# Kernel optimization log

Measured on AMD Instinct MI355X. Metric: run time of the kernel, lower is better.

The kernel has to match this reference:

```python
import jax, jax.numpy as jnp
import numpy as np

N_NODES = 100000
N_EDGES = 400000
N_GRAPHS = 256
HID = 256
BIO = 512
LAYERS = 3
EPS = 1e-5


def _seg_mean(v, seg, num):
    s = jax.ops.segment_sum(v, seg, num_segments=num)
    c = jax.ops.segment_sum(jnp.ones((v.shape[0], 1), v.dtype), seg, num_segments=num)
    return s / jnp.maximum(c, 1.0)


def setup_inputs() -> dict:
    key = jax.random.key(0)
    ks = jax.random.split(key, 24)
    d = {}
    d['x'] = jax.random.randint(ks[0], (N_NODES,), 0, 8)
    d['edge_index'] = jax.random.randint(ks[1], (2, N_EDGES), 0, N_NODES)
    d['edge_attr'] = jax.random.normal(ks[2], (N_EDGES, 4), jnp.float32)
    d['batch'] = jnp.sort(jax.random.randint(ks[3], (N_NODES,), 0, N_GRAPHS))
    sc = 0.06  # ~1/sqrt(HID)
    d['node_emb_W'] = jax.random.normal(ks[4], (8, HID), jnp.float32) * sc
    d['edge_emb_W'] = jax.random.normal(ks[5], (4, HID), jnp.float32) * 0.5
    d['edge_emb_b'] = jnp.zeros((HID,), jnp.float32)
    d['edge_mlp_W1'] = jax.random.normal(ks[6], (HID, HID), jnp.float32) * sc
    d['edge_mlp_b1'] = jnp.zeros((HID,), jnp.float32)
    d['edge_mlp_W2'] = jax.random.normal(ks[7], (HID, HID), jnp.float32) * sc
    d['edge_mlp_b2'] = jnp.zeros((HID,), jnp.float32)
    d['struct_scale'] = jnp.asarray(1.5, jnp.float32)
    d['conv_W1'] = jax.random.normal(ks[8], (LAYERS, HID, HID), jnp.float32) * sc
    d['conv_b1'] = jnp.zeros((LAYERS, HID), jnp.float32)
    d['conv_W2'] = jax.random.normal(ks[9], (LAYERS, HID, HID), jnp.float32) * sc
    d['conv_b2'] = jnp.zeros((LAYERS, HID), jnp.float32)
    d['conv_eps'] = jnp.zeros((LAYERS,), jnp.float32)
    d['norm_gamma'] = jnp.ones((LAYERS, HID), jnp.float32)
    d['norm_beta'] = jnp.zeros((LAYERS, HID), jnp.float32)
    d['norm_alpha'] = jnp.ones((LAYERS, HID), jnp.float32)
    d['mean_bio'] = jax.random.normal(ks[10], (BIO,), jnp.float32)
    d['head_W1'] = jax.random.normal(ks[11], (HID + BIO, HID), jnp.float32) * 0.036
    d['head_b1'] = jnp.zeros((HID,), jnp.float32)
    d['head_W2'] = jax.random.normal(ks[12], (HID, 1), jnp.float32) * sc
    d['head_b2'] = jnp.zeros((1,), jnp.float32)
    return d


def reference(x, edge_index, edge_attr, batch, node_emb_W, edge_emb_W, edge_emb_b,
              edge_mlp_W1, edge_mlp_b1, edge_mlp_W2, edge_mlp_b2, struct_scale,
              conv_W1, conv_b1, conv_W2, conv_b2, conv_eps,
              norm_gamma, norm_beta, norm_alpha, mean_bio,
              head_W1, head_b1, head_W2, head_b2):
    h = node_emb_W[x]  # [N, HID]
    src, dst = edge_index[0], edge_index[1]

    e = edge_attr @ edge_emb_W + edge_emb_b  # edge_emb
    e = jax.nn.relu(e @ edge_mlp_W1 + edge_mlp_b1) @ edge_mlp_W2 + edge_mlp_b2
    struct_mask = edge_attr[:, 1] > 0
    e = e * jnp.where(struct_mask, struct_scale, 1.0)[:, None]

    for l in range(LAYERS):
        # GINE conv: aggregate relu(x_j + e_ij) at target, then 2-layer MLP
        msg = jax.nn.relu(h[src] + e)  # [E, HID]
        agg = jax.ops.segment_sum(msg, dst, num_segments=N_NODES)
        z = (1.0 + conv_eps[l]) * h + agg
        h = jax.nn.relu(z @ conv_W1[l] + conv_b1[l]) @ conv_W2[l] + conv_b2[l]
        # GraphNorm per graph
        mean = _seg_mean(h, batch, N_GRAPHS)  # [G, HID]
        hc = h - norm_alpha[l] * mean[batch]
        var = _seg_mean(hc * hc, batch, N_GRAPHS)
        h = norm_gamma[l] * hc * jax.lax.rsqrt(var[batch] + EPS) + norm_beta[l]

    g = _seg_mean(h, batch, N_GRAPHS)  # global mean pool [G, HID]
    b_emb = jnp.broadcast_to(mean_bio, (g.shape[0], BIO))
    combined = jnp.concatenate([g, b_emb], axis=1)
    out = jax.nn.relu(combined @ head_W1 + head_b1) @ head_W2 + head_b2
    return out.mean(axis=1, keepdims=True)
```

## Files before the change

kernel.cpp:

```cpp
#include <hip/hip_runtime.h>
#include <cstddef>

#define NN 100000
#define NE 400000
#define NG 256
#define HIDC 256
#define EPSN 1e-5f

typedef unsigned short bfu;
using short8 = __attribute__((ext_vector_type(8))) short;
using f32x4  = __attribute__((ext_vector_type(4))) float;
using f32x2  = __attribute__((ext_vector_type(2))) float;

#if defined(__has_builtin)
#if __has_builtin(__builtin_amdgcn_cvt_pk_fp8_f32) && __has_builtin(__builtin_amdgcn_cvt_pk_f32_fp8)
#define HWFP8 1
#endif
#endif

__device__ __forceinline__ float bf2f(bfu b) {
    union { unsigned int u; float f; } v; v.u = ((unsigned int)b) << 16; return v.f;
}
__device__ __forceinline__ bfu f2bf(float f) {
    union { float f; unsigned int u; } v; v.f = f;
    unsigned int r = v.u + 0x7FFFu + ((v.u >> 16) & 1u);
    return (bfu)(r >> 16);
}
__device__ __forceinline__ float e4m3f_sw(unsigned char b) {
    unsigned s = ((unsigned)(b & 0x80u)) << 24;
    unsigned E = (b >> 3) & 15u, M = b & 7u;
    union { unsigned x; float f; } o;
    if (E == 0) { o.f = (float)M * 0.001953125f; o.x |= s; }
    else o.x = s | ((E + 120u) << 23) | (M << 20);
    return o.f;
}
__device__ __forceinline__ unsigned char f2e4m3_sw(float f) {
    union { float f; unsigned u; } v; v.f = f;
    unsigned s = (v.u >> 24) & 0x80u;
    float a = fabsf(f);
    if (!(a < 448.f)) return (unsigned char)(s | 0x7Eu);
    if (a < 0.0009765625f) return (unsigned char)s;
    if (a < 0.015625f) {
        int m = (int)(a * 512.f + 0.5f);
        if (m >= 8) return (unsigned char)(s | 0x08u);
        return (unsigned char)(s | (unsigned)m);
    }
    unsigned u = v.u;
    unsigned r = u + 0x7FFFFu + ((u >> 20) & 1u);
    int E = (int)((r >> 23) & 255u) - 127 + 7;
    unsigned M = (r >> 20) & 7u;
    if (E >= 16) return (unsigned char)(s | 0x7Eu);
    if (E <= 0) {
        int m = (int)(a * 512.f + 0.5f); if (m > 7) m = 7;
        return (unsigned char)(s | (unsigned)m);
    }
    return (unsigned char)(s | ((unsigned)E << 3) | M);
}
__device__ __forceinline__ unsigned int fp8enc4(float a, float b, float c, float d) {
#ifdef HWFP8
    int lo = __builtin_amdgcn_cvt_pk_fp8_f32(a, b, 0, false);
    int hi = __builtin_amdgcn_cvt_pk_fp8_f32(c, d, 0, false);
    return (unsigned int)((lo & 0xFFFF) | (hi << 16));
#else
    return (unsigned)f2e4m3_sw(a) | ((unsigned)f2e4m3_sw(b) << 8) |
           ((unsigned)f2e4m3_sw(c) << 16) | ((unsigned)f2e4m3_sw(d) << 24);
#endif
}
__device__ __forceinline__ float4 fp8dec4(unsigned int u) {
#ifdef HWFP8
    f32x2 lo = __builtin_amdgcn_cvt_pk_f32_fp8((int)u, false);
    f32x2 hi = __builtin_amdgcn_cvt_pk_f32_fp8((int)u, true);
    return make_float4(lo[0], lo[1], hi[0], hi[1]);
#else
    return make_float4(e4m3f_sw(u & 255u), e4m3f_sw((u >> 8) & 255u),
                       e4m3f_sw((u >> 16) & 255u), e4m3f_sw((u >> 24) & 255u));
#endif
}
__device__ __forceinline__ float4 ld4(const void* p, size_t i, int bf) {
    if (bf) {
        ushort4 u = *(const ushort4*)((const bfu*)p + i);
        return make_float4(bf2f(u.x), bf2f(u.y), bf2f(u.z), bf2f(u.w));
    }
    return *(const float4*)((const float*)p + i);
}
__device__ __forceinline__ float ld1(const void* p, size_t i, int bf) {
    return bf ? bf2f(((const bfu*)p)[i]) : ((const float*)p)[i];
}
__device__ __forceinline__ void st1(void* p, size_t i, float v, int bf) {
    if (bf) ((bfu*)p)[i] = f2bf(v); else ((float*)p)[i] = v;
}

__global__ void k_dt2(const unsigned int* __restrict__ g, int* __restrict__ flag) {
    if (threadIdx.x == 0)
        flag[0] = (g[0] == 0x3F800000u) ? 0 : 1;
}

__global__ void k_st2(const int* __restrict__ batch, int* __restrict__ starts) {
    int g = threadIdx.x;
    if (g > NG) return;
    if (g == NG) { starts[NG] = NN; return; }
    int lo = 0, hi = NN;
    while (lo < hi) { int mid = (lo + hi) >> 1; if (batch[mid] < g) lo = mid + 1; else hi = mid; }
    starts[g] = lo;
}

__global__ void k_zi(int* __restrict__ p, int n) {
    int i = blockIdx.x * blockDim.x + threadIdx.x;
    if (i < n) p[i] = 0;
}

__global__ void k_cnt(const int* __restrict__ ei, int* __restrict__ deg) {
    int e = blockIdx.x * blockDim.x + threadIdx.x;
    if (e >= NE) return;
    int d = ei[NE + e];
    if ((unsigned)d < (unsigned)NN) atomicAdd(&deg[d], 1);
}
__global__ void k_sc1(const int* __restrict__ deg, int* __restrict__ rowp,
                      int* __restrict__ part) {
    __shared__ int sh[256];
    int b = blockIdx.x, t = threadIdx.x;
    int i = b * 256 + t;
    int v = (i < NN) ? deg[i] : 0;
    sh[t] = v; __syncthreads();
    for (int off = 1; off < 256; off <<= 1) {
        int add = (t >= off) ? sh[t - off] : 0;
        __syncthreads();
        sh[t] += add; __syncthreads();
    }
    if (i < NN) rowp[i] = sh[t] - v;
    if (t == 255) part[b] = sh[255];
}
__global__ void k_sc2(int* __restrict__ part, int nb) {
    if (threadIdx.x != 0) return;
    int run = 0;
    for (int b = 0; b < nb; ++b) { int t = part[b]; part[b] = run; run += t; }
}
__global__ void k_sc3(int* __restrict__ rowp, const int* __restrict__ part) {
    int i = blockIdx.x * blockDim.x + threadIdx.x;
    if (i < NN) rowp[i] += part[blockIdx.x];
    if (i == 0) rowp[NN] = NE;
}
__global__ void k_cpi(const int* __restrict__ a, int* __restrict__ b, int n) {
    int i = blockIdx.x * blockDim.x + threadIdx.x;
    if (i < n) b[i] = a[i];
}
__global__ void k_fil(const int* __restrict__ ei, int* __restrict__ cursor,
                      int* __restrict__ csrc, int* __restrict__ ceid) {
    int e = blockIdx.x * blockDim.x + threadIdx.x;
    if (e >= NE) return;
    int s = ei[e], d = ei[NE + e];
    if ((unsigned)d >= (unsigned)NN) return;
    int pos = atomicAdd(&cursor[d], 1);
    csrc[pos] = ((unsigned)s < (unsigned)NN) ? s : 0;
    ceid[pos] = e;
}

__global__ void k_wef(const void* __restrict__ Wemb, const void* __restrict__ bemb,
                      const void* __restrict__ W1, const void* __restrict__ b1,
                      float* __restrict__ weff, float* __restrict__ beff,
                      const int* __restrict__ dtf) {
    int bf = *dtf;
    int j = blockIdx.x;
    int n = threadIdx.x;
    float acc = 0.f;
    if (j < 4) {
        for (int k = 0; k < HIDC; ++k)
            acc += ld1(Wemb, (size_t)j * HIDC + k, bf) * ld1(W1, (size_t)k * HIDC + n, bf);
        weff[j * HIDC + n] = acc;
    } else {
        for (int k = 0; k < HIDC; ++k)
            acc += ld1(bemb, k, bf) * ld1(W1, (size_t)k * HIDC + n, bf);
        beff[n] = acc + ld1(b1, n, bf);
    }
}

__device__ __forceinline__ void acc8(float* a, uint4 hv, uint2 ev) {
    float4 e0 = fp8dec4(ev.x);
    float4 e1 = fp8dec4(ev.y);
    a[0] += fmaxf(bf2f((bfu)(hv.x & 0xFFFFu)) + e0.x, 0.f);
    a[1] += fmaxf(bf2f((bfu)(hv.x >> 16))    + e0.y, 0.f);
    a[2] += fmaxf(bf2f((bfu)(hv.y & 0xFFFFu)) + e0.z, 0.f);
    a[3] += fmaxf(bf2f((bfu)(hv.y >> 16))    + e0.w, 0.f);
    a[4] += fmaxf(bf2f((bfu)(hv.z & 0xFFFFu)) + e1.x, 0.f);
    a[5] += fmaxf(bf2f((bfu)(hv.z >> 16))    + e1.y, 0.f);
    a[6] += fmaxf(bf2f((bfu)(hv.w & 0xFFFFu)) + e1.z, 0.f);
    a[7] += fmaxf(bf2f((bfu)(hv.w >> 16))    + e1.w, 0.f);
}
__global__ void k_gat4(const bfu* __restrict__ h, const unsigned char* __restrict__ e8,
                       const int* __restrict__ rowp, const int* __restrict__ csrc,
                       bfu* __restrict__ agg) {
    int tid = blockIdx.x * blockDim.x + threadIdx.x;
    if (tid >= NN * 32) return;
    int n = tid >> 5, q = (tid & 31) << 3;
    int s0 = rowp[n], s1 = rowp[n + 1];
    float a[8] = {};
    int i = s0;
    for (; i + 2 <= s1; i += 2) {
        int src0 = csrc[i], src1 = csrc[i + 1];
        uint4 h0 = *(const uint4*)(h + (size_t)src0 * HIDC + q);
        uint4 h1 = *(const uint4*)(h + (size_t)src1 * HIDC + q);
        uint2 e0 = *(const uint2*)(e8 + (size_t)i * HIDC + q);
        uint2 e1 = *(const uint2*)(e8 + (size_t)(i + 1) * HIDC + q);
        acc8(a, h0, e0);
        acc8(a, h1, e1);
    }
    if (i < s1) {
        int src0 = csrc[i];
        uint4 h0 = *(const uint4*)(h + (size_t)src0 * HIDC + q);
        uint2 e0 = *(const uint2*)(e8 + (size_t)i * HIDC + q);
        acc8(a, h0, e0);
    }
    ushort4 o0, o1;
    o0.x = f2bf(a[0]); o0.y = f2bf(a[1]); o0.z = f2bf(a[2]); o0.w = f2bf(a[3]);
    o1.x = f2bf(a[4]); o1.y = f2bf(a[5]); o1.z = f2bf(a[6]); o1.w = f2bf(a[7]);
    *(ushort4*)(agg + (size_t)n * HIDC + q) = o0;
    *(ushort4*)(agg + (size_t)n * HIDC + q + 4) = o1;
}

__global__ void k_wtr(const void* __restrict__ W, long wOff, bfu* __restrict__ Wt,
                      const int* __restrict__ dtf) {
    int o = blockIdx.x * blockDim.x + threadIdx.x;
    if (o >= HIDC * HIDC) return;
    int blk = o >> 9, pos = o & 511;
    int w = blk >> 5, rem = blk & 31;
    int t = rem >> 3, kb = rem & 7;
    int pr = pos >> 3, j = pos & 7;
    int lr = pr >> 2, lq = pr & 3;
    int n = w * 64 + t * 16 + lr;
    int k = kb * 32 + lq * 8 + j;
    Wt[o] = f2bf(ld1(W, (size_t)wOff + (size_t)k * HIDC + n, *dtf));
}

__global__ void k_emb(const int* __restrict__ x, const void* __restrict__ W,
                      bfu* __restrict__ h, const int* __restrict__ dtf) {
    int tid = blockIdx.x * blockDim.x + threadIdx.x;
    if (tid >= NN * 64) return;
    int bf = *dtf;
    int n = tid >> 6, q = (tid & 63) << 2;
    int xv = x[n]; if ((unsigned)xv >= 8u) xv = 0;
    float4 v = ld4(W, (size_t)xv * HIDC + q, bf);
    ushort4 o; o.x = f2bf(v.x); o.y = f2bf(v.y); o.z = f2bf(v.z); o.w = f2bf(v.w);
    *(ushort4*)(h + (size_t)n * HIDC + q) = o;
}

__global__ __launch_bounds__(512, 8)
void k_me(const void* __restrict__ attrs,
          const float* __restrict__ weff, const float* __restrict__ beff,
          const bfu* __restrict__ Wt, const void* __restrict__ bias,
          const void* __restrict__ scalep,
          unsigned char* __restrict__ C,
          const int* __restrict__ dtf, const int* __restrict__ eidx) {
    __shared__ bfu As[4][64 * 32];
    __shared__ float wsh[1280];
    __shared__ float sf[64];
    const int bf = *dtf;
    const int tid = threadIdx.x;
    const int wave = tid >> 6, lane = tid & 63;
    const int lr = lane & 15, lq = lane >> 4;
    const int wr = wave >> 2, wc = wave & 3;
    const int m0 = blockIdx.x * 64;
    const int row = tid >> 3;
    const int a4 = (tid & 7) << 2;

    for (int v = tid; v < 1280; v += 512)
        wsh[v] = (v < 1024) ? weff[v] : beff[v - 1024];

    float aa[4];
    {
        long er = (long)eidx[m0 + row];
        aa[0] = ld1(attrs, (size_t)er * 4 + 0, bf);
        aa[1] = ld1(attrs, (size_t)er * 4 + 1, bf);
        aa[2] = ld1(attrs, (size_t)er * 4 + 2, bf);
        aa[3] = ld1(attrs, (size_t)er * 4 + 3, bf);
    }
    if ((tid & 7) == 0)
        sf[row] = (aa[1] > 0.f) ? ld1(scalep, 0, bf) : 1.0f;
    __syncthreads();

    f32x4 acc[2][4] = {};
    const bfu* wb = Wt + ((size_t)wc * 32) * 512 + (size_t)(lr * 4 + lq) * 8;

    for (int h = 0; h < 2; ++h) {
        if (h) __syncthreads();
#pragma unroll
        for (int q = 0; q < 4; ++q) {
            const int c = h * 128 + q * 32 + a4;
            float4 bb = *(const float4*)(wsh + 1024 + c);
            float v0 = bb.x, v1 = bb.y, v2 = bb.z, v3 = bb.w;
#pragma unroll
            for (int j = 0; j < 4; ++j) {
                float4 w0 = *(const float4*)(wsh + j * 256 + c);
                v0 += aa[j] * w0.x; v1 += aa[j] * w0.y;
                v2 += aa[j] * w0.z; v3 += aa[j] * w0.w;
            }
            ushort4 o;
            o.x = f2bf(fmaxf(v0, 0.f)); o.y = f2bf(fmaxf(v1, 0.f));
            o.z = f2bf(fmaxf(v2, 0.f)); o.w = f2bf(fmaxf(v3, 0.f));
            *(ushort4*)(&As[q][row * 32 + a4]) = o;
        }
        __syncthreads();
#pragma unroll
        for (int q = 0; q < 4; ++q) {
            const int kb = h * 4 + q;
            short8 fa0 = *(const short8*)(&As[q][(wr * 32 + lr) * 32 + lq * 8]);
            short8 fa1 = *(const short8*)(&As[q][(wr * 32 + 16 + lr) * 32 + lq * 8]);
#pragma unroll
            for (int t = 0; t < 4; ++t) {
                short8 fb = *(const short8*)(wb + (size_t)(t * 8 + kb) * 512);
                acc[0][t] = __builtin_amdgcn_mfma_f32_16x16x32_bf16(fa0, fb, acc[0][t], 0, 0, 0);
                acc[1][t] = __builtin_amdgcn_mfma_f32_16x16x32_bf16(fa1, fb, acc[1][t], 0, 0, 0);
            }
        }
    }
    __syncthreads();

    unsigned char* tile = (unsigned char*)&As[0][0];
    float bv[4];
#pragma unroll
    for (int t = 0; t < 4; ++t)
        bv[t] = ld1(bias, (size_t)(wc * 64 + t * 16 + lr), bf);
#pragma unroll
    for (int r = 0; r < 2; ++r) {
#pragma unroll
        for (int i = 0; i < 4; ++i) {
            int rr = wr * 32 + r * 16 + lq * 4 + i;
            float rs = sf[rr];
            float ov0 = (acc[r][0][i] + bv[0]) * rs;
            float ov1 = (acc[r][1][i] + bv[1]) * rs;
            float ov2 = (acc[r][2][i] + bv[2]) * rs;
            float ov3 = (acc[r][3][i] + bv[3]) * rs;
            unsigned int pk = fp8enc4(ov0, ov1, ov2, ov3);
            int cb = rr * 256 + wc * 64 + lr;
            tile[cb]      = (unsigned char)(pk & 255u);
            tile[cb + 16] = (unsigned char)((pk >> 8) & 255u);
            tile[cb + 32] = (unsigned char)((pk >> 16) & 255u);
            tile[cb + 48] = (unsigned char)(pk >> 24);
        }
    }
    __syncthreads();
    {
        const uint4* lsrc = (const uint4*)(tile + tid * 32);
        uint4 w0 = lsrc[0];
        uint4 w1 = lsrc[1];
        uint4* gdst = (uint4*)(C + (size_t)m0 * HIDC + (size_t)tid * 32);
        gdst[0] = w0;
        gdst[1] = w1;
    }
}

__global__ __launch_bounds__(256)
void k_cnv(bfu* __restrict__ h, const bfu* __restrict__ agg,
           const void* __restrict__ eps, int epsIdx,
           const bfu* __restrict__ Wt1, const void* __restrict__ bias1, long b1Off,
           const bfu* __restrict__ Wt2, const void* __restrict__ bias2, long b2Off,
           const int* __restrict__ dtf) {
    __shared__ bfu Ts[8][64 * 32];
    const int bf = *dtf;
    const int tid = threadIdx.x;
    const int wave = tid >> 6, lane = tid & 63;
    const int lr = lane & 15, lq = lane >> 4;
    const int m0 = blockIdx.x * 64;
    const float epsv = 1.0f + ld1(eps, epsIdx, bf);
    const int row = tid >> 2;
    const int ak = (tid & 3) << 3;
    const int gmA = m0 + row;
    const bfu* wb1 = Wt1 + ((size_t)wave * 32) * 512 + (size_t)(lr * 4 + lq) * 8;
    const bfu* wb2 = Wt2 + ((size_t)wave * 32) * 512 + (size_t)(lr * 4 + lq) * 8;

#pragma unroll
    for (int k0 = 0; k0 < 256; k0 += 32) {
        float hv[8] = {}, gv[8] = {};
        if (gmA < NN) {
            ushort4 h0 = *(const ushort4*)(h + (size_t)gmA * HIDC + k0 + ak);
            ushort4 h1 = *(const ushort4*)(h + (size_t)gmA * HIDC + k0 + ak + 4);
            hv[0]=bf2f(h0.x); hv[1]=bf2f(h0.y); hv[2]=bf2f(h0.z); hv[3]=bf2f(h0.w);
            hv[4]=bf2f(h1.x); hv[5]=bf2f(h1.y); hv[6]=bf2f(h1.z); hv[7]=bf2f(h1.w);
            ushort4 g0 = *(const ushort4*)(agg + (size_t)gmA * HIDC + k0 + ak);
            ushort4 g1 = *(const ushort4*)(agg + (size_t)gmA * HIDC + k0 + ak + 4);
            gv[0]=bf2f(g0.x); gv[1]=bf2f(g0.y); gv[2]=bf2f(g0.z); gv[3]=bf2f(g0.w);
            gv[4]=bf2f(g1.x); gv[5]=bf2f(g1.y); gv[6]=bf2f(g1.z); gv[7]=bf2f(g1.w);
        }
        ushort4 o0, o1;
        o0.x = f2bf(epsv * hv[0] + gv[0]); o0.y = f2bf(epsv * hv[1] + gv[1]);
        o0.z = f2bf(epsv * hv[2] + gv[2]); o0.w = f2bf(epsv * hv[3] + gv[3]);
        o1.x = f2bf(epsv * hv[4] + gv[4]); o1.y = f2bf(epsv * hv[5] + gv[5]);
        o1.z = f2bf(epsv * hv[6] + gv[6]); o1.w = f2bf(epsv * hv[7] + gv[7]);
        *(ushort4*)(&Ts[k0 >> 5][row * 32 + ak]) = o0;
        *(ushort4*)(&Ts[k0 >> 5][row * 32 + ak + 4]) = o1;
    }
    __syncthreads();

    f32x4 acc[4][4] = {};
#pragma unroll
    for (int kb = 0; kb < 8; ++kb) {
        short8 fa[4], fbv[4];
#pragma unroll
        for (int r = 0; r < 4; ++r)
            fa[r] = *(const short8*)(&Ts[kb][(r * 16 + lr) * 32 + lq * 8]);
#pragma unroll
        for (int t = 0; t < 4; ++t)
            fbv[t] = *(const short8*)(wb1 + (size_t)(t * 8 + kb) * 512);
#pragma unroll
        for (int r = 0; r < 4; ++r)
#pragma unroll
            for (int t = 0; t < 4; ++t)
                acc[r][t] = __builtin_amdgcn_mfma_f32_16x16x32_bf16(
                    fa[r], fbv[t], acc[r][t], 0, 0, 0);
    }
    __syncthreads();

    {
        float bv[4];
#pragma unroll
        for (int t = 0; t < 4; ++t)
            bv[t] = ld1(bias1, (size_t)b1Off + wave * 64 + t * 16 + lr, bf);
        const f32x4 z4 = {0.f, 0.f, 0.f, 0.f};
#pragma unroll
        for (int r = 0; r < 4; ++r) {
#pragma unroll
            for (int i = 0; i < 4; ++i) {
                int rowo = r * 16 + lq * 4 + i;
#pragma unroll
                for (int t = 0; t < 4; ++t) {
                    int kk = wave * 64 + t * 16 + lr;
                    Ts[kk >> 5][rowo * 32 + (kk & 31)] =
                        f2bf(fmaxf(acc[r][t][i] + bv[t], 0.f));
                }
            }
        }
#pragma unroll
        for (int r = 0; r < 4; ++r)
#pragma unroll
            for (int t = 0; t < 4; ++t)
                acc[r][t] = z4;
    }
    __syncthreads();

#pragma unroll
    for (int kb = 0; kb < 8; ++kb) {
        short8 fa[4], fbv[4];
#pragma unroll
        for (int r = 0; r < 4; ++r)
            fa[r] = *(const short8*)(&Ts[kb][(r * 16 + lr) * 32 + lq * 8]);
#pragma unroll
        for (int t = 0; t < 4; ++t)
            fbv[t] = *(const short8*)(wb2 + (size_t)(t * 8 + kb) * 512);
#pragma unroll
        for (int r = 0; r < 4; ++r)
#pragma unroll
            for (int t = 0; t < 4; ++t)
                acc[r][t] = __builtin_amdgcn_mfma_f32_16x16x32_bf16(
                    fa[r], fbv[t], acc[r][t], 0, 0, 0);
    }
    float bv[4];
#pragma unroll
    for (int t = 0; t < 4; ++t)
        bv[t] = ld1(bias2, (size_t)b2Off + wave * 64 + t * 16 + lr, bf);
#pragma unroll
    for (int r = 0; r < 4; ++r) {
#pragma unroll
        for (int i = 0; i < 4; ++i) {
            int gm = m0 + r * 16 + lq * 4 + i;
            if (gm >= NN) continue;
            size_t cbase = (size_t)gm * HIDC + wave * 64 + lr;
#pragma unroll
            for (int t = 0; t < 4; ++t)
                h[cbase + t * 16] = f2bf(acc[r][t][i] + bv[t]);
        }
    }
}

__global__ void k_s1(const bfu* __restrict__ h, const int* __restrict__ starts,
                     float* __restrict__ psum, float* __restrict__ psq) {
    int g = blockIdx.x, c8 = blockIdx.y, c = threadIdx.x;
    int s = starts[g], t = starts[g + 1];
    int len = t - s;
    int b = s + (int)(((long)len * c8) >> 3);
    int e = s + (int)(((long)len * (c8 + 1)) >> 3);
    float sum = 0.f, sq = 0.f;
    for (int n = b; n < e; ++n) {
        float v = bf2f(h[(size_t)n * HIDC + c]);
        sum += v; sq += v * v;
    }
    psum[((size_t)g * 8 + c8) * HIDC + c] = sum;
    psq[((size_t)g * 8 + c8) * HIDC + c] = sq;
}
__global__ void k_s2(const int* __restrict__ starts,
                     const float* __restrict__ psum, const float* __restrict__ psq,
                     const void* __restrict__ alpha, long aOff,
                     float* __restrict__ gmean, float* __restrict__ gvar,
                     const int* __restrict__ dtf) {
    int g = blockIdx.x, c = threadIdx.x;
    float sum = 0.f, sq = 0.f;
#pragma unroll
    for (int j = 0; j < 8; ++j) {
        sum += psum[((size_t)g * 8 + j) * HIDC + c];
        sq  += psq[((size_t)g * 8 + j) * HIDC + c];
    }
    int cn = starts[g + 1] - starts[g]; if (cn < 1) cn = 1;
    float cnt = (float)cn;
    float m = sum / cnt;
    float a = ld1(alpha, (size_t)aOff + c, *dtf);
    gmean[g * HIDC + c] = m;
    gvar[g * HIDC + c] = fmaxf(sq / cnt - (2.f * a - a * a) * m * m, 0.f);
}

__global__ void k_nrm(bfu* __restrict__ h, const int* __restrict__ batch,
                      const float* __restrict__ gmean, const float* __restrict__ gvar,
                      const void* __restrict__ gamma, const void* __restrict__ beta,
                      const void* __restrict__ alpha, long pOff,
                      const int* __restrict__ dtf) {
    int tid = blockIdx.x * blockDim.x + threadIdx.x;
    if (tid >= NN * 64) return;
    int bf = *dtf;
    int n = tid >> 6, q = (tid & 63) << 2;
    int g = batch[n]; if ((unsigned)g >= (unsigned)NG) g = 0;
    ushort4 hu = *(ushort4*)(h + (size_t)n * HIDC + q);
    const float4 mv = *(const float4*)(gmean + g * HIDC + q);
    const float4 vv = *(const float4*)(gvar + g * HIDC + q);
    float4 ga = ld4(gamma, (size_t)pOff + q, bf);
    float4 be = ld4(beta, (size_t)pOff + q, bf);
    float4 al = ld4(alpha, (size_t)pOff + q, bf);
    float4 v;
    v.x = ga.x * (bf2f(hu.x) - al.x * mv.x) * rsqrtf(vv.x + EPSN) + be.x;
    v.y = ga.y * (bf2f(hu.y) - al.y * mv.y) * rsqrtf(vv.y + EPSN) + be.y;
    v.z = ga.z * (bf2f(hu.z) - al.z * mv.z) * rsqrtf(vv.z + EPSN) + be.z;
    v.w = ga.w * (bf2f(hu.w) - al.w * mv.w) * rsqrtf(vv.w + EPSN) + be.w;
    ushort4 ov; ov.x = f2bf(v.x); ov.y = f2bf(v.y); ov.z = f2bf(v.z); ov.w = f2bf(v.w);
    *(ushort4*)(h + (size_t)n * HIDC + q) = ov;
}

__global__ void k_pl2(const int* __restrict__ starts,
                      const float* __restrict__ gmean, const float* __restrict__ gvar,
                      const void* __restrict__ gamma, const void* __restrict__ beta,
                      const void* __restrict__ alpha, long pOff,
                      float* __restrict__ g, const int* __restrict__ dtf) {
    int bf = *dtf;
    int gb = blockIdx.x, c = threadIdx.x;
    int cn = starts[gb + 1] - starts[gb];
    if (cn <= 0) { g[gb * HIDC + c] = 0.f; return; }
    float m = gmean[gb * HIDC + c];
    float v = gvar[gb * HIDC + c];
    float ga = ld1(gamma, (size_t)pOff + c, bf);
    float be = ld1(beta, (size_t)pOff + c, bf);
    float al = ld1(alpha, (size_t)pOff + c, bf);
    g[gb * HIDC + c] = ga * (1.f - al) * m * rsqrtf(v + EPSN) + be;
}

__global__ void k_hd(const float* __restrict__ g, const void* __restrict__ bio,
                     const void* __restrict__ W1, const void* __restrict__ b1,
                     const void* __restrict__ W2, const void* __restrict__ b2,
                     void* __restrict__ out, const int* __restrict__ dtf) {
    __shared__ float comb[768];
    __shared__ float red[256];
    __shared__ int nanf;
    int bf = *dtf;
    int gb = blockIdx.x, t = threadIdx.x;
    if (t == 0) nanf = 0;
    comb[t] = g[gb * HIDC + t];
    comb[256 + t] = ld1(bio, t, bf);
    comb[512 + t] = ld1(bio, 256 + t, bf);
    __syncthreads();
    float acc = ld1(b1, t, bf);
    for (int k = 0; k < 768; ++k) acc += comb[k] * ld1(W1, (size_t)k * HIDC + t, bf);
    if (isnan(acc) || isinf(acc)) nanf = 1;
    float hid = fmaxf(acc, 0.f);
    red[t] = hid * ld1(W2, t, bf);
    __syncthreads();
    for (int off = 128; off > 0; off >>= 1) {
        if (t < off) red[t] += red[t + off];
        __syncthreads();
    }
    if (t == 0) {
        float r = red[0] + ld1(b2, 0, bf);
        if (nanf || isnan(r)) r = 999.0f;
        st1(out, gb, r, bf);
    }
}

extern "C" void kernel_launch(void* const* d_in, const int* in_sizes, int n_in,
                              void* d_out, int out_size, void* d_ws, size_t ws_size,
                              hipStream_t stream) {
    const int* x = (const int*)d_in[0];
    const int* ei = (const int*)d_in[1];
    const void* eattr = d_in[2];
    const int* batch = (const int*)d_in[3];
    const void* node_emb_W = d_in[4];
    const void* edge_emb_W = d_in[5];
    const void* edge_emb_b = d_in[6];
    const void* emlp_W1 = d_in[7];
    const void* emlp_b1 = d_in[8];
    const void* emlp_W2 = d_in[9];
    const void* emlp_b2 = d_in[10];
    const void* struct_scale = d_in[11];
    const void* conv_W1 = d_in[12];
    const void* conv_b1 = d_in[13];
    const void* conv_W2 = d_in[14];
    const void* conv_b2 = d_in[15];
    const void* conv_eps = d_in[16];
    const void* ngamma = d_in[17];
    const void* nbeta = d_in[18];
    const void* nalpha = d_in[19];
    const void* mean_bio = d_in[20];
    const void* head_W1 = d_in[21];
    const void* head_b1 = d_in[22];
    const void* head_W2 = d_in[23];
    const void* head_b2 = d_in[24];
    (void)in_sizes; (void)n_in; (void)out_size; (void)ws_size;

    const size_t H_B = (size_t)NN * HIDC * 2;
    const size_t E8_B = (size_t)NE * HIDC;
    char* p = (char*)d_ws;
    bfu* hbuf = (bfu*)p; p += H_B;
    bfu* aggb = (bfu*)p; p += H_B;
    unsigned char* e8 = (unsigned char*)p; p += E8_B;
    bfu* wt = (bfu*)p; p += 8 * 65536 * 2;
    int* rowp = (int*)p;
    int* cursor = rowp + 100352;
    int* part = cursor + 100352;
    int* splits = part + 1024;
    int* cnts = splits + 8;
    int* csrc = cnts + 8;
    int* ceid = csrc + NE;
    p = (char*)(ceid + NE);
    float* psum = (float*)p; p += (size_t)NG * 8 * HIDC * 4;
    float* psq = (float*)p; p += (size_t)NG * 8 * HIDC * 4;
    char* small = p;
    int* starts = (int*)small;
    int* dtf = (int*)(small + 2048);
    float* weff = (float*)(small + 4096);
    float* beff = weff + 4 * HIDC;
    float* gmean = (float*)(small + 16384);
    float* gvar = gmean + NG * HIDC;
    float* gpool = gvar + NG * HIDC;
    (void)splits; (void)cnts;

    k_dt2<<<1, 64, 0, stream>>>((const unsigned int*)ngamma, dtf);
    k_st2<<<1, 512, 0, stream>>>(batch, starts);
    k_emb<<<(NN * 64 + 255) / 256, 256, 0, stream>>>(x, node_emb_W, hbuf, dtf);
    k_wef<<<5, 256, 0, stream>>>(edge_emb_W, edge_emb_b, emlp_W1, emlp_b1,
                                 weff, beff, dtf);

    k_wtr<<<256, 256, 0, stream>>>(emlp_W2, 0, wt + 65536, dtf);
    for (int l = 0; l < 3; ++l) {
        k_wtr<<<256, 256, 0, stream>>>(conv_W1, (long)l * HIDC * HIDC, wt + (2 + l) * 65536, dtf);
        k_wtr<<<256, 256, 0, stream>>>(conv_W2, (long)l * HIDC * HIDC, wt + (5 + l) * 65536, dtf);
    }

    const int NBN = (NN + 255) / 256;
    k_zi<<<NBN, 256, 0, stream>>>(cursor, NN);
    k_cnt<<<(NE + 255) / 256, 256, 0, stream>>>(ei, cursor);
    k_sc1<<<NBN, 256, 0, stream>>>(cursor, rowp, part);
    k_sc2<<<1, 64, 0, stream>>>(part, NBN);
    k_sc3<<<NBN, 256, 0, stream>>>(rowp, part);
    k_cpi<<<NBN, 256, 0, stream>>>(rowp, cursor, NN);
    k_fil<<<(NE + 255) / 256, 256, 0, stream>>>(ei, cursor, csrc, ceid);

    dim3 gE((NE + 63) / 64), gN((NN + 63) / 64);
    k_me<<<gE, 512, 0, stream>>>(eattr, weff, beff, wt + 65536, emlp_b2,
                                 struct_scale, e8, dtf, ceid);

    dim3 gS1(NG, 8);
    const int gatBlocks = (NN * 32 + 255) / 256;

    for (int l = 0; l < 3; ++l) {
        k_gat4<<<gatBlocks, 256, 0, stream>>>(hbuf, e8, rowp, csrc, aggb);
        k_cnv<<<gN, 256, 0, stream>>>(
            hbuf, aggb, conv_eps, l,
            wt + (2 + l) * 65536, conv_b1, (long)l * HIDC,
            wt + (5 + l) * 65536, conv_b2, (long)l * HIDC, dtf);
        k_s1<<<gS1, 256, 0, stream>>>(hbuf, starts, psum, psq);
        k_s2<<<NG, 256, 0, stream>>>(starts, psum, psq, nalpha, (long)l * HIDC,
                                     gmean, gvar, dtf);
        if (l < 2) {
            k_nrm<<<(NN * 64 + 255) / 256, 256, 0, stream>>>(
                hbuf, batch, gmean, gvar, ngamma, nbeta, nalpha, (long)l * HIDC, dtf);
        }
    }

    k_pl2<<<NG, 256, 0, stream>>>(starts, gmean, gvar, ngamma, nbeta, nalpha,
                                  (long)2 * HIDC, gpool, dtf);
    k_hd<<<NG, 256, 0, stream>>>(gpool, mean_bio, head_W1, head_b1,
                                 head_W2, head_b2, d_out, dtf);
}
```

Before: 977.1 us.

## Fuse edge gather-aggregation into conv MLP kernel with ping-pong h buffers

Removes the separate gather kernel and computes the neighbour aggregation directly inside the conv kernel while building the shared-memory A tile, so the intermediate agg buffer is never written to or read back from global memory. Because other blocks still read the old h during the gather, the kernel writes to a second h buffer and the two are swapped each layer. Each thread now walks its node's edge list twice (once per 128-column half) and holds 32 float accumulators. That raises register pressure and keeps divergent, latency-bound edge loops inside the GEMM kernel, which can stall the MFMA work and lower occupancy.

```diff
diff --git a/kernel.cpp b/kernel.cpp
--- a/kernel.cpp
+++ b/kernel.cpp
@@ -185,36 +185,6 @@
     a[5] += fmaxf(bf2f((bfu)(hv.z >> 16))    + e1.y, 0.f);
     a[6] += fmaxf(bf2f((bfu)(hv.w & 0xFFFFu)) + e1.z, 0.f);
     a[7] += fmaxf(bf2f((bfu)(hv.w >> 16))    + e1.w, 0.f);
-}
-__global__ void k_gat4(const bfu* __restrict__ h, const unsigned char* __restrict__ e8,
-                       const int* __restrict__ rowp, const int* __restrict__ csrc,
-                       bfu* __restrict__ agg) {
-    int tid = blockIdx.x * blockDim.x + threadIdx.x;
-    if (tid >= NN * 32) return;
-    int n = tid >> 5, q = (tid & 31) << 3;
-    int s0 = rowp[n], s1 = rowp[n + 1];
-    float a[8] = {};
-    int i = s0;
-    for (; i + 2 <= s1; i += 2) {
-        int src0 = csrc[i], src1 = csrc[i + 1];
-        uint4 h0 = *(const uint4*)(h + (size_t)src0 * HIDC + q);
-        uint4 h1 = *(const uint4*)(h + (size_t)src1 * HIDC + q);
-        uint2 e0 = *(const uint2*)(e8 + (size_t)i * HIDC + q);
-        uint2 e1 = *(const uint2*)(e8 + (size_t)(i + 1) * HIDC + q);
-        acc8(a, h0, e0);
-        acc8(a, h1, e1);
-    }
-    if (i < s1) {
-        int src0 = csrc[i];
-        uint4 h0 = *(const uint4*)(h + (size_t)src0 * HIDC + q);
-        uint2 e0 = *(const uint2*)(e8 + (size_t)i * HIDC + q);
-        acc8(a, h0, e0);
-    }
-    ushort4 o0, o1;
-    o0.x = f2bf(a[0]); o0.y = f2bf(a[1]); o0.z = f2bf(a[2]); o0.w = f2bf(a[3]);
-    o1.x = f2bf(a[4]); o1.y = f2bf(a[5]); o1.z = f2bf(a[6]); o1.w = f2bf(a[7]);
-    *(ushort4*)(agg + (size_t)n * HIDC + q) = o0;
-    *(ushort4*)(agg + (size_t)n * HIDC + q + 4) = o1;
 }
 
 __global__ void k_wtr(const void* __restrict__ W, long wOff, bfu* __restrict__ Wt,
@@ -349,11 +319,13 @@
 }
 
 __global__ __launch_bounds__(256)
-void k_cnv(bfu* __restrict__ h, const bfu* __restrict__ agg,
-           const void* __restrict__ eps, int epsIdx,
-           const bfu* __restrict__ Wt1, const void* __restrict__ bias1, long b1Off,
-           const bfu* __restrict__ Wt2, const void* __restrict__ bias2, long b2Off,
-           const int* __restrict__ dtf) {
+void k_cnv2(const bfu* __restrict__ hin, bfu* __restrict__ hout,
+            const unsigned char* __restrict__ e8,
+            const int* __restrict__ rowp, const int* __restrict__ csrc,
+            const void* __restrict__ eps, int epsIdx,
+            const bfu* __restrict__ Wt1, const void* __restrict__ bias1, long b1Off,
+            const bfu* __restrict__ Wt2, const void* __restrict__ bias2, long b2Off,
+            const int* __restrict__ dtf) {
     __shared__ bfu Ts[8][64 * 32];
     const int bf = *dtf;
     const int tid = threadIdx.x;
@@ -367,26 +339,41 @@
     const bfu* wb1 = Wt1 + ((size_t)wave * 32) * 512 + (size_t)(lr * 4 + lq) * 8;
     const bfu* wb2 = Wt2 + ((size_t)wave * 32) * 512 + (size_t)(lr * 4 + lq) * 8;
 
-#pragma unroll
-    for (int k0 = 0; k0 < 256; k0 += 32) {
-        float hv[8] = {}, gv[8] = {};
-        if (gmA < NN) {
-            ushort4 h0 = *(const ushort4*)(h + (size_t)gmA * HIDC + k0 + ak);
-            ushort4 h1 = *(const ushort4*)(h + (size_t)gmA * HIDC + k0 + ak + 4);
-            hv[0]=bf2f(h0.x); hv[1]=bf2f(h0.y); hv[2]=bf2f(h0.z); hv[3]=bf2f(h0.w);
-            hv[4]=bf2f(h1.x); hv[5]=bf2f(h1.y); hv[6]=bf2f(h1.z); hv[7]=bf2f(h1.w);
-            ushort4 g0 = *(const ushort4*)(agg + (size_t)gmA * HIDC + k0 + ak);
-            ushort4 g1 = *(const ushort4*)(agg + (size_t)gmA * HIDC + k0 + ak + 4);
-            gv[0]=bf2f(g0.x); gv[1]=bf2f(g0.y); gv[2]=bf2f(g0.z); gv[3]=bf2f(g0.w);
-            gv[4]=bf2f(g1.x); gv[5]=bf2f(g1.y); gv[6]=bf2f(g1.z); gv[7]=bf2f(g1.w);
-        }
-        ushort4 o0, o1;
-        o0.x = f2bf(epsv * hv[0] + gv[0]); o0.y = f2bf(epsv * hv[1] + gv[1]);
-        o0.z = f2bf(epsv * hv[2] + gv[2]); o0.w = f2bf(epsv * hv[3] + gv[3]);
-        o1.x = f2bf(epsv * hv[4] + gv[4]); o1.y = f2bf(epsv * hv[5] + gv[5]);
-        o1.z = f2bf(epsv * hv[6] + gv[6]); o1.w = f2bf(epsv * hv[7] + gv[7]);
-        *(ushort4*)(&Ts[k0 >> 5][row * 32 + ak]) = o0;
-        *(ushort4*)(&Ts[k0 >> 5][row * 32 + ak + 4]) = o1;
+    int es0 = 0, es1 = 0;
+    if (gmA < NN) { es0 = rowp[gmA]; es1 = rowp[gmA + 1]; }
+
+#pragma unroll
+    for (int gq = 0; gq < 2; ++gq) {
+        float a[32] = {};
+        const int cbase = gq * 128 + ak;
+        for (int i = es0; i < es1; ++i) {
+            int src = csrc[i];
+            const bfu* hp = hin + (size_t)src * HIDC + cbase;
+            const unsigned char* ep = e8 + (size_t)i * HIDC + cbase;
+#pragma unroll
+            for (int t4 = 0; t4 < 4; ++t4) {
+                uint4 hv = *(const uint4*)(hp + t4 * 32);
+                uint2 ev = *(const uint2*)(ep + t4 * 32);
+                acc8(a + t4 * 8, hv, ev);
+            }
+        }
+#pragma unroll
+        for (int t4 = 0; t4 < 4; ++t4) {
+            float hv[8] = {};
+            if (gmA < NN) {
+                ushort4 h0 = *(const ushort4*)(hin + (size_t)gmA * HIDC + cbase + t4 * 32);
+                ushort4 h1 = *(const ushort4*)(hin + (size_t)gmA * HIDC + cbase + t4 * 32 + 4);
+                hv[0]=bf2f(h0.x); hv[1]=bf2f(h0.y); hv[2]=bf2f(h0.z); hv[3]=bf2f(h0.w);
+                hv[4]=bf2f(h1.x); hv[5]=bf2f(h1.y); hv[6]=bf2f(h1.z); hv[7]=bf2f(h1.w);
+            }
+            ushort4 o0, o1;
+            o0.x = f2bf(epsv * hv[0] + a[t4*8+0]); o0.y = f2bf(epsv * hv[1] + a[t4*8+1]);
+            o0.z = f2bf(epsv * hv[2] + a[t4*8+2]); o0.w = f2bf(epsv * hv[3] + a[t4*8+3]);
+            o1.x = f2bf(epsv * hv[4] + a[t4*8+4]); o1.y = f2bf(epsv * hv[5] + a[t4*8+5]);
+            o1.z = f2bf(epsv * hv[6] + a[t4*8+6]); o1.w = f2bf(epsv * hv[7] + a[t4*8+7]);
+            *(ushort4*)(&Ts[gq * 4 + t4][row * 32 + ak]) = o0;
+            *(ushort4*)(&Ts[gq * 4 + t4][row * 32 + ak + 4]) = o1;
+        }
     }
     __syncthreads();
 
@@ -465,7 +452,7 @@
             size_t cbase = (size_t)gm * HIDC + wave * 64 + lr;
 #pragma unroll
             for (int t = 0; t < 4; ++t)
-                h[cbase + t * 16] = f2bf(acc[r][t][i] + bv[t]);
+                hout[cbase + t * 16] = f2bf(acc[r][t][i] + bv[t]);
         }
     }
 }
@@ -612,7 +599,7 @@
     const size_t E8_B = (size_t)NE * HIDC;
     char* p = (char*)d_ws;
     bfu* hbuf = (bfu*)p; p += H_B;
-    bfu* aggb = (bfu*)p; p += H_B;
+    bfu* h2 = (bfu*)p; p += H_B;
     unsigned char* e8 = (unsigned char*)p; p += E8_B;
     bfu* wt = (bfu*)p; p += 8 * 65536 * 2;
     int* rowp = (int*)p;
@@ -661,21 +648,22 @@
                                  struct_scale, e8, dtf, ceid);
 
     dim3 gS1(NG, 8);
-    const int gatBlocks = (NN * 32 + 255) / 256;
-
+
+    bfu* hin = hbuf;
+    bfu* hout = h2;
     for (int l = 0; l < 3; ++l) {
-        k_gat4<<<gatBlocks, 256, 0, stream>>>(hbuf, e8, rowp, csrc, aggb);
-        k_cnv<<<gN, 256, 0, stream>>>(
-            hbuf, aggb, conv_eps, l,
+        k_cnv2<<<gN, 256, 0, stream>>>(
+            hin, hout, e8, rowp, csrc, conv_eps, l,
             wt + (2 + l) * 65536, conv_b1, (long)l * HIDC,
             wt + (5 + l) * 65536, conv_b2, (long)l * HIDC, dtf);
-        k_s1<<<gS1, 256, 0, stream>>>(hbuf, starts, psum, psq);
+        k_s1<<<gS1, 256, 0, stream>>>(hout, starts, psum, psq);
         k_s2<<<NG, 256, 0, stream>>>(starts, psum, psq, nalpha, (long)l * HIDC,
                                      gmean, gvar, dtf);
         if (l < 2) {
             k_nrm<<<(NN * 64 + 255) / 256, 256, 0, stream>>>(
-                hbuf, batch, gmean, gvar, ngamma, nbeta, nalpha, (long)l * HIDC, dtf);
-        }
+                hout, batch, gmean, gvar, ngamma, nbeta, nalpha, (long)l * HIDC, dtf);
+        }
+        bfu* tmp = hin; hin = hout; hout = tmp;
     }
 
     k_pl2<<<NG, 256, 0, stream>>>(starts, gmean, gvar, ngamma, nbeta, nalpha,
```

New measurement: 1.003 ms. 1.03x slower.

## Fuse GraphNorm per-graph sum/sumsq reduction into conv MLP epilogue via atomics

Applied to the files above, without the earlier changes.

Moves the per-graph sum and sum-of-squares accumulation out of the separate k_s1 pass and into the k_cnv epilogue. Tiles whose 64 rows all belong to one graph reduce in registers and with shuffles, then issue one atomic per column. Mixed tiles fall back to per-element atomics. This avoids re-reading the full hidden tensor after each layer, at the cost of a zeroing launch, float atomics with nondeterministic summation order, and extra epilogue work.

```diff
diff --git a/kernel.cpp b/kernel.cpp
--- a/kernel.cpp
+++ b/kernel.cpp
@@ -350,9 +350,11 @@
 
 __global__ __launch_bounds__(256)
 void k_cnv(bfu* __restrict__ h, const bfu* __restrict__ agg,
+           const int* __restrict__ batch,
            const void* __restrict__ eps, int epsIdx,
            const bfu* __restrict__ Wt1, const void* __restrict__ bias1, long b1Off,
            const bfu* __restrict__ Wt2, const void* __restrict__ bias2, long b2Off,
+           float* __restrict__ psum, float* __restrict__ psq,
            const int* __restrict__ dtf) {
     __shared__ bfu Ts[8][64 * 32];
     const int bf = *dtf;
@@ -456,47 +458,70 @@
 #pragma unroll
     for (int t = 0; t < 4; ++t)
         bv[t] = ld1(bias2, (size_t)b2Off + wave * 64 + t * 16 + lr, bf);
-#pragma unroll
-    for (int r = 0; r < 4; ++r) {
-#pragma unroll
-        for (int i = 0; i < 4; ++i) {
-            int gm = m0 + r * 16 + lq * 4 + i;
-            if (gm >= NN) continue;
-            size_t cbase = (size_t)gm * HIDC + wave * 64 + lr;
-#pragma unroll
-            for (int t = 0; t < 4; ++t)
-                h[cbase + t * 16] = f2bf(acc[r][t][i] + bv[t]);
-        }
-    }
-}
-
-__global__ void k_s1(const bfu* __restrict__ h, const int* __restrict__ starts,
-                     float* __restrict__ psum, float* __restrict__ psq) {
-    int g = blockIdx.x, c8 = blockIdx.y, c = threadIdx.x;
-    int s = starts[g], t = starts[g + 1];
-    int len = t - s;
-    int b = s + (int)(((long)len * c8) >> 3);
-    int e = s + (int)(((long)len * (c8 + 1)) >> 3);
-    float sum = 0.f, sq = 0.f;
-    for (int n = b; n < e; ++n) {
-        float v = bf2f(h[(size_t)n * HIDC + c]);
-        sum += v; sq += v * v;
-    }
-    psum[((size_t)g * 8 + c8) * HIDC + c] = sum;
-    psq[((size_t)g * 8 + c8) * HIDC + c] = sq;
-}
+
+    int lastRow = m0 + 63; if (lastRow >= NN) lastRow = NN - 1;
+    const int g0 = batch[m0 < NN ? m0 : NN - 1];
+    const int g1 = batch[lastRow];
+    const bool fast = (g0 == g1) && (m0 + 63 < NN);
+
+    if (fast) {
+        float st[4] = {0.f, 0.f, 0.f, 0.f};
+        float sq[4] = {0.f, 0.f, 0.f, 0.f};
+#pragma unroll
+        for (int r = 0; r < 4; ++r) {
+#pragma unroll
+            for (int i = 0; i < 4; ++i) {
+                int gm = m0 + r * 16 + lq * 4 + i;
+                size_t cbase = (size_t)gm * HIDC + wave * 64 + lr;
+#pragma unroll
+                for (int t = 0; t < 4; ++t) {
+                    float o = acc[r][t][i] + bv[t];
+                    h[cbase + t * 16] = f2bf(o);
+                    st[t] += o; sq[t] += o * o;
+                }
+            }
+        }
+#pragma unroll
+        for (int t = 0; t < 4; ++t) {
+            float s = st[t], q = sq[t];
+            s += __shfl_xor(s, 16); q += __shfl_xor(q, 16);
+            s += __shfl_xor(s, 32); q += __shfl_xor(q, 32);
+            if (lq == 0) {
+                int c = wave * 64 + t * 16 + lr;
+                atomicAdd(&psum[(size_t)g0 * HIDC + c], s);
+                atomicAdd(&psq[(size_t)g0 * HIDC + c], q);
+            }
+        }
+    } else {
+#pragma unroll
+        for (int r = 0; r < 4; ++r) {
+#pragma unroll
+            for (int i = 0; i < 4; ++i) {
+                int gm = m0 + r * 16 + lq * 4 + i;
+                if (gm >= NN) continue;
+                int g = batch[gm];
+                size_t cbase = (size_t)gm * HIDC + wave * 64 + lr;
+#pragma unroll
+                for (int t = 0; t < 4; ++t) {
+                    float o = acc[r][t][i] + bv[t];
+                    h[cbase + t * 16] = f2bf(o);
+                    int c = wave * 64 + t * 16 + lr;
+                    atomicAdd(&psum[(size_t)g * HIDC + c], o);
+                    atomicAdd(&psq[(size_t)g * HIDC + c], o * o);
+                }
+            }
+        }
+    }
+}
+
 __global__ void k_s2(const int* __restrict__ starts,
                      const float* __restrict__ psum, const float* __restrict__ psq,
                      const void* __restrict__ alpha, long aOff,
                      float* __restrict__ gmean, float* __restrict__ gvar,
                      const int* __restrict__ dtf) {
     int g = blockIdx.x, c = threadIdx.x;
-    float sum = 0.f, sq = 0.f;
-#pragma unroll
-    for (int j = 0; j < 8; ++j) {
-        sum += psum[((size_t)g * 8 + j) * HIDC + c];
-        sq  += psq[((size_t)g * 8 + j) * HIDC + c];
-    }
+    float sum = psum[(size_t)g * HIDC + c];
+    float sq  = psq[(size_t)g * HIDC + c];
     int cn = starts[g + 1] - starts[g]; if (cn < 1) cn = 1;
     float cnt = (float)cn;
     float m = sum / cnt;
@@ -624,7 +649,8 @@
     int* ceid = csrc + NE;
     p = (char*)(ceid + NE);
     float* psum = (float*)p; p += (size_t)NG * 8 * HIDC * 4;
-    float* psq = (float*)p; p += (size_t)NG * 8 * HIDC * 4;
+    float* psq = psum + NG * HIDC;
+    p += (size_t)NG * 8 * HIDC * 4;
     char* small = p;
     int* starts = (int*)small;
     int* dtf = (int*)(small + 2048);
@@ -660,16 +686,17 @@
     k_me<<<gE, 512, 0, stream>>>(eattr, weff, beff, wt + 65536, emlp_b2,
                                  struct_scale, e8, dtf, ceid);
 
-    dim3 gS1(NG, 8);
     const int gatBlocks = (NN * 32 + 255) / 256;
+    const int ZB = (2 * NG * HIDC + 255) / 256;
 
     for (int l = 0; l < 3; ++l) {
         k_gat4<<<gatBlocks, 256, 0, stream>>>(hbuf, e8, rowp, csrc, aggb);
+        k_zi<<<ZB, 256, 0, stream>>>((int*)psum, 2 * NG * HIDC);
         k_cnv<<<gN, 256, 0, stream>>>(
-            hbuf, aggb, conv_eps, l,
+            hbuf, aggb, batch, conv_eps, l,
             wt + (2 + l) * 65536, conv_b1, (long)l * HIDC,
-            wt + (5 + l) * 65536, conv_b2, (long)l * HIDC, dtf);
-        k_s1<<<gS1, 256, 0, stream>>>(hbuf, starts, psum, psq);
+            wt + (5 + l) * 65536, conv_b2, (long)l * HIDC,
+            psum, psq, dtf);
         k_s2<<<NG, 256, 0, stream>>>(starts, psum, psq, nalpha, (long)l * HIDC,
                                      gmean, gvar, dtf);
         if (l < 2) {
```

Result: slower. 1.136 ms (+16.3%).
